# Performance work log

Hardware: AMD Instinct MI355X
Metric: run time of the kernel (lower is better)

Reference implementation:

```python
import jax, jax.numpy as jnp
import numpy as np

GROUP_SIZE = 128

def setup_inputs() -> dict:
    key = jax.random.key(0)
    k1, k2, k3, k4 = jax.random.split(key, 4)
    in_f, out_f = 4096, 4096
    num_groups = (in_f + GROUP_SIZE - 1) // GROUP_SIZE  # 32
    x = jax.random.normal(k1, (4, 2048, in_f), dtype=jnp.float32)
    qweight = jax.random.randint(k2, (out_f, in_f), 0, 16, dtype=jnp.int32)
    scales = jax.random.uniform(k3, (out_f, num_groups), dtype=jnp.float32)
    bias = jax.random.normal(k4, (out_f,), dtype=jnp.float32)
    return {"x": x, "qweight": qweight, "scales": scales, "bias": bias}

def reference(x, qweight, scales, bias):
    out_f, in_f = qweight.shape
    # group-wise dequantize: broadcast each per-group scale over its columns
    scale_full = jnp.repeat(scales, GROUP_SIZE, axis=1)[:, :in_f]  # [out, in]
    weight = qweight.astype(scales.dtype) * scale_full             # [out, in]
    # F.linear(x, weight, bias) == x @ weight.T + bias
    return jnp.einsum('bsi,oi->bso', x, weight) + bias
```

## Files before the change

### kernel.cpp

```cpp
#include <hip/hip_runtime.h>
#include <hip/hip_bf16.h>

typedef __bf16 bf16_t;
typedef __bf16 bf16x8 __attribute__((ext_vector_type(8)));
typedef float  f32x4  __attribute__((ext_vector_type(4)));
typedef int    i32x4  __attribute__((ext_vector_type(4)));

static constexpr int M_ = 8192;
static constexpr int N_ = 4096;
static constexpr int K_ = 4096;

static constexpr int BM = 256, BN = 256, BK = 64;
static constexpr int NT = K_ / BK;
static constexpr int HT_ELEMS  = 128 * 64;
static constexpr int BUF_ELEMS = 2 * HT_ELEMS;

__device__ __forceinline__ void load_lds16(const bf16_t* g, bf16_t* l) {
  __builtin_amdgcn_global_load_lds(
      (const __attribute__((address_space(1))) void*)g,
      (__attribute__((address_space(3))) void*)l,
      16, 0, 0);
}

#define MFMA16(a, b, c) __builtin_amdgcn_mfma_f32_16x16x32_bf16((a), (b), (c), 0, 0, 0)

__global__ __launch_bounds__(256) void cvt_x_kernel(const float* __restrict__ x,
                                                    bf16_t* __restrict__ xb) {
  const size_t i = ((size_t)blockIdx.x * 256 + threadIdx.x) * 8;
  const f32x4 f0 = __builtin_nontemporal_load((const f32x4*)(x + i));
  const f32x4 f1 = __builtin_nontemporal_load((const f32x4*)(x + i + 4));
  bf16x8 o;
  o[0] = (bf16_t)f0[0]; o[1] = (bf16_t)f0[1]; o[2] = (bf16_t)f0[2]; o[3] = (bf16_t)f0[3];
  o[4] = (bf16_t)f1[0]; o[5] = (bf16_t)f1[1]; o[6] = (bf16_t)f1[2]; o[7] = (bf16_t)f1[3];
  *(bf16x8*)(xb + i) = o;
}

__global__ __launch_bounds__(256) void dequant_kernel(const int* __restrict__ q,
                                                      const float* __restrict__ s,
                                                      bf16_t* __restrict__ wb) {
  const size_t base = ((size_t)blockIdx.x * 256 + threadIdx.x) * 8;
  const int o  = (int)(base >> 12);
  const int ii = (int)(base & 4095);
  const float sc = s[(o << 5) + (ii >> 7)];
  const i32x4 q0 = __builtin_nontemporal_load((const i32x4*)(q + base));
  const i32x4 q1 = __builtin_nontemporal_load((const i32x4*)(q + base + 4));
  bf16x8 w;
  w[0] = (bf16_t)((float)q0[0] * sc); w[1] = (bf16_t)((float)q0[1] * sc);
  w[2] = (bf16_t)((float)q0[2] * sc); w[3] = (bf16_t)((float)q0[3] * sc);
  w[4] = (bf16_t)((float)q1[0] * sc); w[5] = (bf16_t)((float)q1[1] * sc);
  w[6] = (bf16_t)((float)q1[2] * sc); w[7] = (bf16_t)((float)q1[3] * sc);
  *(bf16x8*)(wb + base) = w;
}

__global__ __launch_bounds__(512, 2) void gemm_kernel(const bf16_t* __restrict__ A,
                                                      const bf16_t* __restrict__ B,
                                                      const float* __restrict__ bias,
                                                      float* __restrict__ C) {
  __shared__ __align__(16) bf16_t As[2 * BUF_ELEMS];
  __shared__ __align__(16) bf16_t Bs[2 * BUF_ELEMS];

  const int tid  = threadIdx.x;
  const int lane = tid & 63;
  const int wave = tid >> 6;
  const int ln = lane & 15;
  const int lq = lane >> 4;
  const int wm = wave >> 2;
  const int wn = wave & 3;

  const int bid = blockIdx.x;
  const int wg  = (bid & 7) * 64 + (bid >> 3);
  const int bn  = (wg & 15) * BN;
  const int bm  = (wg >> 4) * BM;

  const int r_sub = tid >> 3;
  const int g_col = ((tid & 7) ^ (r_sub & 7)) * 8;
  const size_t a_base = (size_t)(bm + r_sub) * K_ + g_col;
  const size_t b_base = (size_t)(bn + r_sub) * K_ + g_col;
  const int lds_off = tid * 8;

  auto stageA = [&](int t, int h) {
    bf16_t* d = As + (t & 1) * BUF_ELEMS + h * HT_ELEMS + lds_off;
    const bf16_t* s = A + a_base + (size_t)(h * 128) * K_ + (size_t)t * BK;
    load_lds16(s, d);
    load_lds16(s + (size_t)64 * K_, d + 4096);
  };
  auto stageB = [&](int t, int h) {
    bf16_t* d = Bs + (t & 1) * BUF_ELEMS + h * HT_ELEMS + lds_off;
    const bf16_t* s = B + b_base + (size_t)(h * 128) * K_ + (size_t)t * BK;
    load_lds16(s, d);
    load_lds16(s + (size_t)64 * K_, d + 4096);
  };

  const int kx0 = (lq * 8) ^ ((ln & 7) * 8);
  const int kx1 = (32 + lq * 8) ^ ((ln & 7) * 8);
  const int a_row_off = (wm * 16 + ln) * 64;
  const int b_row_off = (wn * 32 + ln) * 64;

  f32x4 acc[8][4] = {};

  stageA(0, 0); stageB(0, 0); stageB(0, 1); stageA(0, 1);
  stageA(1, 0); stageB(1, 0); stageB(1, 1);
  asm volatile("s_waitcnt vmcnt(6)" ::: "memory");
  __builtin_amdgcn_s_barrier();

  for (int T = 0; T < NT; ++T) {
    const bf16_t* as = As + (T & 1) * BUF_ELEMS;
    const bf16_t* bs = Bs + (T & 1) * BUF_ELEMS;
    bf16x8 af[4][2], bqA[2][2], bqB[2][2];

#pragma unroll
    for (int i = 0; i < 4; ++i) {
      const bf16_t* p = as + a_row_off + i * 2048;
      af[i][0] = *(const bf16x8*)(p + kx0);
      af[i][1] = *(const bf16x8*)(p + kx1);
    }
#pragma unroll
    for (int j = 0; j < 2; ++j) {
      const bf16_t* p = bs + b_row_off + j * 1024;
      bqA[j][0] = *(const bf16x8*)(p + kx0);
      bqA[j][1] = *(const bf16x8*)(p + kx1);
    }
    if (T + 1 < NT) stageA(T + 1, 1);
    asm volatile("s_waitcnt lgkmcnt(8)" ::: "memory");
    __builtin_amdgcn_s_barrier();
    asm volatile("s_waitcnt lgkmcnt(0)" ::: "memory");
    __builtin_amdgcn_sched_barrier(0);
    __builtin_amdgcn_s_setprio(1);
#pragma unroll
    for (int i = 0; i < 4; ++i)
#pragma unroll
      for (int j = 0; j < 2; ++j) {
        acc[i][j] = MFMA16(af[i][0], bqA[j][0], acc[i][j]);
        acc[i][j] = MFMA16(af[i][1], bqA[j][1], acc[i][j]);
      }
    __builtin_amdgcn_s_setprio(0);
    __builtin_amdgcn_s_barrier();

#pragma unroll
    for (int j = 0; j < 2; ++j) {
      const bf16_t* p = bs + HT_ELEMS + b_row_off + j * 1024;
      bqB[j][0] = *(const bf16x8*)(p + kx0);
      bqB[j][1] = *(const bf16x8*)(p + kx1);
    }
    if (T + 2 < NT) stageA(T + 2, 0);
    __builtin_amdgcn_s_barrier();
    asm volatile("s_waitcnt lgkmcnt(0)" ::: "memory");
    __builtin_amdgcn_sched_barrier(0);
    __builtin_amdgcn_s_setprio(1);
#pragma unroll
    for (int i = 0; i < 4; ++i)
#pragma unroll
      for (int j = 0; j < 2; ++j) {
        acc[i][j + 2] = MFMA16(af[i][0], bqB[j][0], acc[i][j + 2]);
        acc[i][j + 2] = MFMA16(af[i][1], bqB[j][1], acc[i][j + 2]);
      }
    __builtin_amdgcn_s_setprio(0);
    __builtin_amdgcn_s_barrier();

#pragma unroll
    for (int i = 0; i < 4; ++i) {
      const bf16_t* p = as + HT_ELEMS + a_row_off + i * 2048;
      af[i][0] = *(const bf16x8*)(p + kx0);
      af[i][1] = *(const bf16x8*)(p + kx1);
    }
    if (T + 2 < NT) stageB(T + 2, 0);
    __builtin_amdgcn_s_barrier();
    asm volatile("s_waitcnt lgkmcnt(0)" ::: "memory");
    __builtin_amdgcn_sched_barrier(0);
    __builtin_amdgcn_s_setprio(1);
#pragma unroll
    for (int i = 0; i < 4; ++i)
#pragma unroll
      for (int j = 0; j < 2; ++j) {
        acc[i + 4][j + 2] = MFMA16(af[i][0], bqB[j][0], acc[i + 4][j + 2]);
        acc[i + 4][j + 2] = MFMA16(af[i][1], bqB[j][1], acc[i + 4][j + 2]);
      }
    __builtin_amdgcn_s_setprio(0);
    __builtin_amdgcn_s_barrier();

    if (T + 2 < NT) {
      stageB(T + 2, 1);
      asm volatile("s_waitcnt vmcnt(6)" ::: "memory");
    } else {
      asm volatile("s_waitcnt vmcnt(0)" ::: "memory");
    }
    __builtin_amdgcn_s_barrier();
    __builtin_amdgcn_sched_barrier(0);
    __builtin_amdgcn_s_setprio(1);
#pragma unroll
    for (int i = 0; i < 4; ++i)
#pragma unroll
      for (int j = 0; j < 2; ++j) {
        acc[i + 4][j] = MFMA16(af[i][0], bqA[j][0], acc[i + 4][j]);
        acc[i + 4][j] = MFMA16(af[i][1], bqA[j][1], acc[i + 4][j]);
      }
    __builtin_amdgcn_s_setprio(0);
    __builtin_amdgcn_s_barrier();
  }

#pragma unroll
  for (int j = 0; j < 4; ++j) {
    const int col = bn + (j >> 1) * 128 + wn * 32 + (j & 1) * 16 + ln;
    const float bv = bias[col];
#pragma unroll
    for (int i = 0; i < 8; ++i) {
      const int row0 = bm + (i >> 2) * 128 + (i & 3) * 32 + wm * 16 + lq * 4;
      float* cp = C + (size_t)row0 * N_ + col;
#pragma unroll
      for (int r = 0; r < 4; ++r) {
        __builtin_nontemporal_store(acc[i][j][r] + bv, cp);
        cp += N_;
      }
    }
  }
}

extern "C" void kernel_launch(void* const* d_in, const int* in_sizes, int n_in,
                              void* d_out, int out_size, void* d_ws, size_t ws_size,
                              hipStream_t stream) {
  const float* x    = (const float*)d_in[0];
  const int*   qw   = (const int*)d_in[1];
  const float* sc   = (const float*)d_in[2];
  const float* bias = (const float*)d_in[3];
  float* out = (float*)d_out;

  bf16_t* xb = (bf16_t*)d_ws;
  bf16_t* wb = xb + (size_t)M_ * K_;

  cvt_x_kernel<<<(int)(((size_t)M_ * K_) / (256 * 8)), 256, 0, stream>>>(x, xb);
  dequant_kernel<<<(int)(((size_t)N_ * K_) / (256 * 8)), 256, 0, stream>>>(qw, sc, wb);

  const int nwg = (N_ / BN) * (M_ / BM);
  gemm_kernel<<<nwg, 512, 0, stream>>>(xb, wb, bias, out);
}
```

Baseline: 471.1 us.

## Fuse fp32-to-bf16 conversion and dequantization into the GEMM main loop

Removes the separate convert and dequant kernels. The GEMM now loads fp32 activations and int32 weights directly into registers, converts and scales them, and writes bf16 into LDS. This cuts the round trip of writing and rereading bf16 intermediates plus two kernel launches. In exchange it gives up the asynchronous global-to-LDS loads, doubles global read bytes per tile, and raises register pressure. It also changes workgroup-to-tile mapping so each XCD covers an 8x8 block of tiles.

Result: slower. 1.270 ms (+169.6%).

```diff
diff --git a/kernel.cpp b/kernel.cpp
--- a/kernel.cpp
+++ b/kernel.cpp
@@ -15,45 +15,11 @@
 static constexpr int HT_ELEMS  = 128 * 64;
 static constexpr int BUF_ELEMS = 2 * HT_ELEMS;
 
-__device__ __forceinline__ void load_lds16(const bf16_t* g, bf16_t* l) {
-  __builtin_amdgcn_global_load_lds(
-      (const __attribute__((address_space(1))) void*)g,
-      (__attribute__((address_space(3))) void*)l,
-      16, 0, 0);
-}
-
 #define MFMA16(a, b, c) __builtin_amdgcn_mfma_f32_16x16x32_bf16((a), (b), (c), 0, 0, 0)
 
-__global__ __launch_bounds__(256) void cvt_x_kernel(const float* __restrict__ x,
-                                                    bf16_t* __restrict__ xb) {
-  const size_t i = ((size_t)blockIdx.x * 256 + threadIdx.x) * 8;
-  const f32x4 f0 = __builtin_nontemporal_load((const f32x4*)(x + i));
-  const f32x4 f1 = __builtin_nontemporal_load((const f32x4*)(x + i + 4));
-  bf16x8 o;
-  o[0] = (bf16_t)f0[0]; o[1] = (bf16_t)f0[1]; o[2] = (bf16_t)f0[2]; o[3] = (bf16_t)f0[3];
-  o[4] = (bf16_t)f1[0]; o[5] = (bf16_t)f1[1]; o[6] = (bf16_t)f1[2]; o[7] = (bf16_t)f1[3];
-  *(bf16x8*)(xb + i) = o;
-}
-
-__global__ __launch_bounds__(256) void dequant_kernel(const int* __restrict__ q,
-                                                      const float* __restrict__ s,
-                                                      bf16_t* __restrict__ wb) {
-  const size_t base = ((size_t)blockIdx.x * 256 + threadIdx.x) * 8;
-  const int o  = (int)(base >> 12);
-  const int ii = (int)(base & 4095);
-  const float sc = s[(o << 5) + (ii >> 7)];
-  const i32x4 q0 = __builtin_nontemporal_load((const i32x4*)(q + base));
-  const i32x4 q1 = __builtin_nontemporal_load((const i32x4*)(q + base + 4));
-  bf16x8 w;
-  w[0] = (bf16_t)((float)q0[0] * sc); w[1] = (bf16_t)((float)q0[1] * sc);
-  w[2] = (bf16_t)((float)q0[2] * sc); w[3] = (bf16_t)((float)q0[3] * sc);
-  w[4] = (bf16_t)((float)q1[0] * sc); w[5] = (bf16_t)((float)q1[1] * sc);
-  w[6] = (bf16_t)((float)q1[2] * sc); w[7] = (bf16_t)((float)q1[3] * sc);
-  *(bf16x8*)(wb + base) = w;
-}
-
-__global__ __launch_bounds__(512, 2) void gemm_kernel(const bf16_t* __restrict__ A,
-                                                      const bf16_t* __restrict__ B,
+__global__ __launch_bounds__(512, 2) void gemm_kernel(const float* __restrict__ X,
+                                                      const int* __restrict__ Q,
+                                                      const float* __restrict__ S,
                                                       const float* __restrict__ bias,
                                                       float* __restrict__ C) {
   __shared__ __align__(16) bf16_t As[2 * BUF_ELEMS];
@@ -67,29 +33,75 @@
   const int wm = wave >> 2;
   const int wn = wave & 3;
 
-  const int bid = blockIdx.x;
-  const int wg  = (bid & 7) * 64 + (bid >> 3);
-  const int bn  = (wg & 15) * BN;
-  const int bm  = (wg >> 4) * BM;
+  const int bid   = blockIdx.x;
+  const int xcd   = bid & 7;
+  const int local = bid >> 3;
+  const int bm = (((xcd >> 1) << 3) + (local >> 3)) * BM;
+  const int bn = (((xcd & 1) << 3) + (local & 7)) * BN;
 
   const int r_sub = tid >> 3;
   const int g_col = ((tid & 7) ^ (r_sub & 7)) * 8;
-  const size_t a_base = (size_t)(bm + r_sub) * K_ + g_col;
-  const size_t b_base = (size_t)(bn + r_sub) * K_ + g_col;
   const int lds_off = tid * 8;
 
-  auto stageA = [&](int t, int h) {
-    bf16_t* d = As + (t & 1) * BUF_ELEMS + h * HT_ELEMS + lds_off;
-    const bf16_t* s = A + a_base + (size_t)(h * 128) * K_ + (size_t)t * BK;
-    load_lds16(s, d);
-    load_lds16(s + (size_t)64 * K_, d + 4096);
-  };
-  auto stageB = [&](int t, int h) {
-    bf16_t* d = Bs + (t & 1) * BUF_ELEMS + h * HT_ELEMS + lds_off;
-    const bf16_t* s = B + b_base + (size_t)(h * 128) * K_ + (size_t)t * BK;
-    load_lds16(s, d);
-    load_lds16(s + (size_t)64 * K_, d + 4096);
-  };
+  const float* Xb[4];
+  const int*   Qb[4];
+  const float* Sb[4];
+#pragma unroll
+  for (int hc = 0; hc < 4; ++hc) {
+    const int roff = (hc >> 1) * 128 + (hc & 1) * 64 + r_sub;
+    Xb[hc] = X + (size_t)(bm + roff) * K_ + g_col;
+    Qb[hc] = Q + (size_t)(bn + roff) * K_ + g_col;
+    Sb[hc] = S + (size_t)(bn + roff) * 32;
+  }
+
+  f32x4 aL[4][2];
+  i32x4 bL[4][2];
+  float sc4[4];
+
+#define ISSUE_A(T1)                                                            \
+  _Pragma("unroll")                                                            \
+  for (int hc = 0; hc < 4; ++hc) {                                             \
+    const float* p = Xb[hc] + (size_t)(T1) * BK;                               \
+    aL[hc][0] = *(const f32x4*)(p);                                            \
+    aL[hc][1] = *(const f32x4*)(p + 4);                                        \
+  }
+
+#define ISSUE_SB(T1)                                                           \
+  _Pragma("unroll")                                                            \
+  for (int hc = 0; hc < 4; ++hc) sc4[hc] = Sb[hc][(T1) >> 1];                  \
+  _Pragma("unroll")                                                            \
+  for (int hc = 0; hc < 4; ++hc) {                                             \
+    const int* p = Qb[hc] + (size_t)(T1) * BK;                                 \
+    bL[hc][0] = *(const i32x4*)(p);                                            \
+    bL[hc][1] = *(const i32x4*)(p + 4);                                        \
+  }
+
+#define CVT_WRITE_A(T1)                                                        \
+  _Pragma("unroll")                                                            \
+  for (int hc = 0; hc < 4; ++hc) {                                             \
+    bf16x8 w;                                                                  \
+    _Pragma("unroll")                                                          \
+    for (int v = 0; v < 4; ++v) {                                              \
+      w[v]     = (bf16_t)aL[hc][0][v];                                         \
+      w[v + 4] = (bf16_t)aL[hc][1][v];                                         \
+    }                                                                          \
+    *(bf16x8*)(As + ((T1) & 1) * BUF_ELEMS + (hc >> 1) * HT_ELEMS +            \
+               (hc & 1) * 4096 + lds_off) = w;                                 \
+  }
+
+#define CVT_WRITE_B(T1)                                                        \
+  _Pragma("unroll")                                                            \
+  for (int hc = 0; hc < 4; ++hc) {                                             \
+    const float sc = sc4[hc];                                                  \
+    bf16x8 w;                                                                  \
+    _Pragma("unroll")                                                          \
+    for (int v = 0; v < 4; ++v) {                                              \
+      w[v]     = (bf16_t)((float)bL[hc][0][v] * sc);                           \
+      w[v + 4] = (bf16_t)((float)bL[hc][1][v] * sc);                           \
+    }                                                                          \
+    *(bf16x8*)(Bs + ((T1) & 1) * BUF_ELEMS + (hc >> 1) * HT_ELEMS +            \
+               (hc & 1) * 4096 + lds_off) = w;                                 \
+  }
 
   const int kx0 = (lq * 8) ^ ((ln & 7) * 8);
   const int kx1 = (32 + lq * 8) ^ ((ln & 7) * 8);
@@ -98,15 +110,20 @@
 
   f32x4 acc[8][4] = {};
 
-  stageA(0, 0); stageB(0, 0); stageB(0, 1); stageA(0, 1);
-  stageA(1, 0); stageB(1, 0); stageB(1, 1);
-  asm volatile("s_waitcnt vmcnt(6)" ::: "memory");
+  ISSUE_A(0)
+  ISSUE_SB(0)
+  asm volatile("s_waitcnt vmcnt(12)" ::: "memory");
+  CVT_WRITE_A(0)
+  asm volatile("s_waitcnt vmcnt(0)" ::: "memory");
+  CVT_WRITE_B(0)
+  asm volatile("s_waitcnt lgkmcnt(0)" ::: "memory");
   __builtin_amdgcn_s_barrier();
 
   for (int T = 0; T < NT; ++T) {
     const bf16_t* as = As + (T & 1) * BUF_ELEMS;
     const bf16_t* bs = Bs + (T & 1) * BUF_ELEMS;
     bf16x8 af[4][2], bqA[2][2], bqB[2][2];
+    const bool stage = (T + 1 < NT);
 
 #pragma unroll
     for (int i = 0; i < 4; ++i) {
@@ -120,7 +137,7 @@
       bqA[j][0] = *(const bf16x8*)(p + kx0);
       bqA[j][1] = *(const bf16x8*)(p + kx1);
     }
-    if (T + 1 < NT) stageA(T + 1, 1);
+    if (stage) { ISSUE_A(T + 1) }
     asm volatile("s_waitcnt lgkmcnt(8)" ::: "memory");
     __builtin_amdgcn_s_barrier();
     asm volatile("s_waitcnt lgkmcnt(0)" ::: "memory");
@@ -142,7 +159,7 @@
       bqB[j][0] = *(const bf16x8*)(p + kx0);
       bqB[j][1] = *(const bf16x8*)(p + kx1);
     }
-    if (T + 2 < NT) stageA(T + 2, 0);
+    if (stage) { ISSUE_SB(T + 1) }
     __builtin_amdgcn_s_barrier();
     asm volatile("s_waitcnt lgkmcnt(0)" ::: "memory");
     __builtin_amdgcn_sched_barrier(0);
@@ -163,7 +180,6 @@
       af[i][0] = *(const bf16x8*)(p + kx0);
       af[i][1] = *(const bf16x8*)(p + kx1);
     }
-    if (T + 2 < NT) stageB(T + 2, 0);
     __builtin_amdgcn_s_barrier();
     asm volatile("s_waitcnt lgkmcnt(0)" ::: "memory");
     __builtin_amdgcn_sched_barrier(0);
@@ -176,16 +192,12 @@
         acc[i + 4][j + 2] = MFMA16(af[i][1], bqB[j][1], acc[i + 4][j + 2]);
       }
     __builtin_amdgcn_s_setprio(0);
-    __builtin_amdgcn_s_barrier();
-
-    if (T + 2 < NT) {
-      stageB(T + 2, 1);
-      asm volatile("s_waitcnt vmcnt(6)" ::: "memory");
-    } else {
-      asm volatile("s_waitcnt vmcnt(0)" ::: "memory");
-    }
-    __builtin_amdgcn_s_barrier();
-    __builtin_amdgcn_sched_barrier(0);
+    if (stage) {
+      asm volatile("s_waitcnt vmcnt(12)" ::: "memory");
+      CVT_WRITE_A(T + 1)
+    }
+    __builtin_amdgcn_s_barrier();
+
     __builtin_amdgcn_s_setprio(1);
 #pragma unroll
     for (int i = 0; i < 4; ++i)
@@ -195,6 +207,11 @@
         acc[i + 4][j] = MFMA16(af[i][1], bqA[j][1], acc[i + 4][j]);
       }
     __builtin_amdgcn_s_setprio(0);
+    if (stage) {
+      asm volatile("s_waitcnt vmcnt(0)" ::: "memory");
+      CVT_WRITE_B(T + 1)
+    }
+    asm volatile("s_waitcnt lgkmcnt(0)" ::: "memory");
     __builtin_amdgcn_s_barrier();
   }
 
@@ -213,6 +230,10 @@
       }
     }
   }
+#undef ISSUE_A
+#undef ISSUE_SB
+#undef CVT_WRITE_A
+#undef CVT_WRITE_B
 }
 
 extern "C" void kernel_launch(void* const* d_in, const int* in_sizes, int n_in,
@@ -224,12 +245,6 @@
   const float* bias = (const float*)d_in[3];
   float* out = (float*)d_out;
 
-  bf16_t* xb = (bf16_t*)d_ws;
-  bf16_t* wb = xb + (size_t)M_ * K_;
-
-  cvt_x_kernel<<<(int)(((size_t)M_ * K_) / (256 * 8)), 256, 0, stream>>>(x, xb);
-  dequant_kernel<<<(int)(((size_t)N_ * K_) / (256 * 8)), 256, 0, stream>>>(qw, sc, wb);
-
   const int nwg = (N_ / BN) * (M_ / BM);
-  gemm_kernel<<<nwg, 512, 0, stream>>>(xb, wb, bias, out);
+  gemm_kernel<<<nwg, 512, 0, stream>>>(x, qw, sc, bias, out);
 }
```
